# Kernel optimization log

Hardware: AMD Instinct MI355X
Metric: run time of the kernel (lower is better)

Reference implementation:

```python
import jax, jax.numpy as jnp
import numpy as np

B, M, NV, P = 4, 30000, 300000, 32
CIN, CBEV, NH = 128, 256, 4
HY, WX = 180, 180            # downsampled BEV grid (1440/8)
XSP, YSP, ZSP = 1440, 1440, 40
PC_MIN = np.array([-75.2, -75.2, -2.0], np.float32)
PC_SIZE = np.array([150.4, 150.4, 6.0], np.float32)


def setup_inputs() -> dict:
    key = jax.random.key(0)
    ks = jax.random.split(key, 20)
    w = lambda i, shape: jax.random.normal(ks[i], shape, jnp.float32) * 0.02

    voxel_features = jax.random.normal(ks[0], (NV, CIN), jnp.float32)
    b = jax.random.randint(ks[1], (NV,), 0, B)
    z = jax.random.randint(ks[2], (NV,), 0, ZSP)
    y = jax.random.randint(ks[3], (NV,), 0, YSP)
    x = jax.random.randint(ks[4], (NV,), 0, XSP)
    sp_indices = jnp.stack([b, z, y, x], -1).astype(jnp.int32)  # [NV,4] (b,z,y,x)

    # unique downsampled BEV cells -> deterministic scatter_nd
    cells = jax.random.permutation(ks[5], B * HY * WX)[:M]
    nb = cells // (HY * WX)
    rem = cells % (HY * WX)
    new_indices = jnp.stack([nb, jnp.zeros_like(nb), rem // WX, rem % WX], -1).astype(jnp.int32)

    ki = jax.random.randint(ks[6], (M, P), 0, NV)
    drop = jax.random.uniform(ks[7], (M, P)) < 0.3
    drop = drop.at[:, 0].set(False)  # at least one valid neighbor per query
    key_indices = jnp.where(drop, -1, ki).astype(jnp.int32)

    bev = jax.random.normal(ks[8], (B, CBEV, HY, WX), jnp.float32)

    return {
        'voxel_features': voxel_features, 'sp_indices': sp_indices,
        'new_indices': new_indices, 'key_indices': key_indices, 'bev': bev,
        'w_pos': w(9, (CIN, 3)), 'b_pos': jnp.zeros((CIN,), jnp.float32),
        'w_bev': w(10, (CIN, CBEV)), 'b_bev': jnp.zeros((CIN,), jnp.float32),
        'g_q': jnp.ones((CIN,), jnp.float32), 'be_q': jnp.zeros((CIN,), jnp.float32),
        'g_k': jnp.ones((CIN,), jnp.float32), 'be_k': jnp.zeros((CIN,), jnp.float32),
        'g_f': jnp.ones((CIN,), jnp.float32), 'be_f': jnp.zeros((CIN,), jnp.float32),
        'w_in': w(11, (3 * CIN, CIN)), 'b_in': jnp.zeros((3 * CIN,), jnp.float32),
        'w_out': w(12, (CIN, CIN)), 'b_out': jnp.zeros((CIN,), jnp.float32),
        'w_fc1': w(13, (CIN, CIN)), 'b_fc1': jnp.zeros((CIN,), jnp.float32),
        'w_fc2': w(14, (CIN, CIN)), 'b_fc2': jnp.zeros((CIN,), jnp.float32),
    }


def _ln(x, g, b):
    m = jnp.mean(x, -1, keepdims=True)
    v = jnp.mean((x - m) ** 2, -1, keepdims=True)
    return (x - m) * jax.lax.rsqrt(v + 1e-5) * g + b


def reference(voxel_features, sp_indices, new_indices, key_indices, bev,
              w_pos, b_pos, w_bev, b_bev, g_q, be_q, g_k, be_k, g_f, be_f,
              w_in, b_in, w_out, b_out, w_fc1, b_fc1, w_fc2, b_fc2):
    gelu = lambda t: jax.nn.gelu(t, approximate=False)
    key_mask = key_indices < 0            # [M,P] True -> padded neighbor
    safe = jnp.clip(key_indices, 0)

    key_feats = voxel_features[safe]      # [M,P,CIN] gather (grouping_operation)

    # voxel-center coords (with_coords), xyz order from indices[:, [3,2,1]]
    vs_sp = jnp.asarray(PC_SIZE / np.array([XSP, YSP, ZSP], np.float32))
    sp_coords = (sp_indices[:, jnp.array([3, 2, 1])].astype(jnp.float32) + 0.5) * vs_sp + jnp.asarray(PC_MIN)
    key_coords = sp_coords[safe]          # [M,P,3]
    vs_new = jnp.asarray(PC_SIZE / np.array([HY, WX, 1], np.float32))
    que_coords = (new_indices[:, jnp.array([3, 2, 1])].astype(jnp.float32) + 0.5) * vs_new + jnp.asarray(PC_MIN)
    key_coords = key_coords - que_coords[:, None, :]   # use_relative_coords

    # positional embedding: Conv1d(3, CIN, 1) == linear over coord dim, + GELU
    key_feats = key_feats + gelu(key_coords @ w_pos.T + b_pos)

    # dense BEV gather at downsampled voxel locations
    bev_hw = jnp.transpose(bev, (0, 2, 3, 1))           # [B,HY,WX,CBEV]
    bev_feats = bev_hw[new_indices[:, 0], new_indices[:, 2], new_indices[:, 3]]  # [M,CBEV]

    shortcut = gelu(bev_feats @ w_bev.T + b_bev)        # [M,CIN]  bev_proj
    q = _ln(shortcut, g_q, be_q)
    k = _ln(key_feats, g_k, be_k)                       # [M,P,CIN]

    C, dh = CIN, CIN // NH
    wq, wk, wv = w_in[:C], w_in[C:2 * C], w_in[2 * C:]
    bq, bk, bv = b_in[:C], b_in[C:2 * C], b_in[2 * C:]
    m = q.shape[0]
    qh = (q @ wq.T + bq).reshape(m, NH, dh)             # query seq-len 1 per voxel
    kh = (k @ wk.T + bk).reshape(m, P, NH, dh)
    vh = (k @ wv.T + bv).reshape(m, P, NH, dh)
    scale = jnp.float32(1.0 / np.sqrt(dh))
    logits = jnp.einsum('mhd,mphd->mhp', qh, kh) * scale
    logits = jnp.where(key_mask[:, None, :], -jnp.inf, logits)  # key_padding_mask
    attn = jax.nn.softmax(logits, -1)
    av = jnp.einsum('mhp,mphd->mhd', attn, vh).reshape(m, C)
    attend = av @ w_out.T + b_out

    xf = attend + shortcut
    yf = _ln(xf, g_f, be_f)
    yf = gelu(yf @ w_fc1.T + b_fc1) @ w_fc2.T + b_fc2   # MLP
    feats = yf + xf                                     # [M,CIN]

    # densify: scatter_nd into [B, z=1, HY, WX, C] then -> [B, C, HY, WX]
    dense = jnp.zeros((B, HY, WX, C), feats.dtype)
    dense = dense.at[new_indices[:, 0], new_indices[:, 2], new_indices[:, 3]].set(feats)
    return jnp.transpose(dense, (0, 3, 1, 2))
```

## Files before the change

### kernel.cpp

```cpp
#include <hip/hip_runtime.h>
#include <hip/hip_bf16.h>
#include <cmath>

#define C_IN 128
#define NKEY 32
#define N_H 4
#define D_H 32
#define C_BEV 256
#define H_Y 180
#define W_X 180

typedef __attribute__((ext_vector_type(8))) short short8;
typedef __attribute__((ext_vector_type(4))) float f32x4;

__device__ __forceinline__ float gelu_fast(float x) {
    const float y2 = fminf(1.5957691216057308f * (x + 0.044715f * x * x * x), 80.0f);
    const float e = __expf(y2);
    return x * e / (e + 1.0f);
}
__device__ __forceinline__ float dot4(float4 a, float4 b) {
    return a.x * b.x + a.y * b.y + a.z * b.z + a.w * b.w;
}
__device__ __forceinline__ float bf2f(ushort u) {
    union { unsigned int i; float f; } c; c.i = ((unsigned int)u) << 16; return c.f;
}
__device__ __forceinline__ ushort f2bf(float x) {
    __hip_bfloat16 h = __float2bfloat16(x);
    return *reinterpret_cast<ushort*>(&h);
}

__global__ void conv_swz(const float* __restrict__ src, ushort* __restrict__ dst,
                         int K, int total) {
    const int idx = blockIdx.x * 256 + threadIdx.x;
    if (idx < total) {
        const int j = idx & 7;
        const int t8 = idx >> 3;
        const int lane = t8 & 63;
        const int tile = t8 >> 6;
        const int NK = K >> 5;
        const int kt = tile % NK, ct = tile / NK;
        const int row = ct * 16 + (lane & 15);
        const int k = kt * 32 + (lane >> 4) * 8 + j;
        dst[idx] = f2bf(src[(size_t)row * K + k]);
    }
}

__global__ void conv_swz_t(const float* __restrict__ w_in, ushort* __restrict__ dst) {
    const int idx = blockIdx.x * 256 + threadIdx.x;
    if (idx < 16384) {
        const int j = idx & 7;
        const int lane = (idx >> 3) & 63;
        const int tile = idx >> 9;
        const int ct = tile & 7, h = tile >> 3;
        const int row_w = 128 + h * 32 + (lane >> 4) * 8 + j;
        const int col = ct * 16 + (lane & 15);
        dst[idx] = f2bf(w_in[(size_t)row_w * C_IN + col]);
    }
}

__global__ void build_inv(const int* __restrict__ ni, int* __restrict__ inv, int M) {
    const int m = blockIdx.x * 256 + threadIdx.x;
    if (m < M) {
        const int b = ni[m*4+0], y = ni[m*4+2], x = ni[m*4+3];
        inv[(b * H_Y + y) * W_X + x] = m;
    }
}

__global__ __launch_bounds__(256) void compact_bev(
    const float* __restrict__ bev, const int* __restrict__ inv,
    float* __restrict__ pack)
{
    const int bid = blockIdx.x;
    const int xr = bid % 12;
    const int y  = (bid / 12) % H_Y;
    const int b  = bid / (12 * H_Y);
    const int x0 = xr * 16;
    const int width = (x0 + 16 <= W_X) ? 16 : (W_X - x0);
    const int tid = threadIdx.x;

    __shared__ float tile[16][257];

    const int xq = (tid & 3) * 4;
    #pragma unroll
    for (int p = 0; p < 4; ++p) {
        const int c = p * 64 + (tid >> 2);
        if (xq < width) {
            const float4 v = *(const float4*)(bev +
                (((size_t)b * C_BEV + c) * H_Y + y) * W_X + x0 + xq);
            tile[xq+0][c] = v.x; tile[xq+1][c] = v.y;
            tile[xq+2][c] = v.z; tile[xq+3][c] = v.w;
        }
    }
    __syncthreads();
    for (int xi = 0; xi < width; ++xi) {
        const int m = inv[(b * H_Y + y) * W_X + x0 + xi];
        if (m >= 0) pack[(size_t)m * C_BEV + tid] = tile[xi][tid];
    }
}

__global__ __launch_bounds__(256) void write_out_t(
    const int* __restrict__ inv, const float* __restrict__ featbuf,
    float* __restrict__ out)
{
    const int bid = blockIdx.x;
    const int xr = bid % 12;
    const int y  = (bid / 12) % H_Y;
    const int b  = bid / (12 * H_Y);
    const int x0 = xr * 16;
    const int width = (x0 + 16 <= W_X) ? 16 : (W_X - x0);
    const int tid = threadIdx.x;

    __shared__ float tile[16][C_IN + 1];
    __shared__ int m16[16];

    if (tid < 16) m16[tid] = (tid < width) ? inv[(b * H_Y + y) * W_X + x0 + tid] : -1;
    __syncthreads();

    #pragma unroll
    for (int pass = 0; pass < 8; ++pass) {
        const int xi = pass * 2 + (tid >> 7);
        const int c  = tid & 127;
        const int m  = m16[xi];
        tile[xi][c] = (m >= 0) ? featbuf[(size_t)m * C_IN + c] : 0.0f;
    }
    __syncthreads();

    #pragma unroll
    for (int pass = 0; pass < 8; ++pass) {
        const int c  = pass * 16 + (tid >> 4);
        const int xi = tid & 15;
        if (xi < width)
            out[(((size_t)b * C_IN + c) * H_Y + y) * W_X + x0 + xi] = tile[xi][c];
    }
}

__global__ __launch_bounds__(256) void k_pre(
    float* __restrict__ pack, const ushort* __restrict__ wbev_s,
    const float* __restrict__ b_bev, const float* __restrict__ g_q,
    const float* __restrict__ be_q, const ushort* __restrict__ wq_s,
    const ushort* __restrict__ wkt_s, const float* __restrict__ b_in,
    float* __restrict__ sc_g, float* __restrict__ tbvbuf, const int M)
{
    __shared__ ushort bevl16[16][C_BEV + 8];
    __shared__ float  scl[16][C_IN];
    __shared__ ushort qlnl16[16][C_IN + 8];
    __shared__ ushort qhl16[16][C_IN + 8];
    __shared__ ushort tl16[16][N_H][C_IN];
    const int tid = threadIdx.x;
    const int m16 = blockIdx.x * 16;
    const int wave = tid >> 6, lane = tid & 63;
    const int llo = lane & 15, lhi = lane >> 4;
    const int qs = tid >> 4, seg = tid & 15;
    int mq = m16 + qs; if (mq >= M) mq = M - 1;

    {
        const float4* srcp = (const float4*)(pack + (size_t)mq * C_BEV + seg * 16);
        ushort tmp[16];
        #pragma unroll
        for (int j4 = 0; j4 < 4; ++j4) {
            const float4 v = srcp[j4];
            tmp[j4*4+0] = f2bf(v.x); tmp[j4*4+1] = f2bf(v.y);
            tmp[j4*4+2] = f2bf(v.z); tmp[j4*4+3] = f2bf(v.w);
        }
        short8* d = (short8*)&bevl16[qs][seg * 16];
        d[0] = *(short8*)&tmp[0];
        d[1] = *(short8*)&tmp[8];
    }
    __syncthreads();

    {
        f32x4 acc0 = {0.f,0.f,0.f,0.f}, acc1 = {0.f,0.f,0.f,0.f};
        #pragma unroll
        for (int kt = 0; kt < 8; ++kt) {
            const short8 a = *(const short8*)&bevl16[llo][kt*32 + lhi*8];
            const short8 b0 = *(const short8*)&wbev_s[(size_t)(((wave    )*8 + kt)*64 + lane)*8];
            const short8 b1 = *(const short8*)&wbev_s[(size_t)(((wave + 4)*8 + kt)*64 + lane)*8];
            acc0 = __builtin_amdgcn_mfma_f32_16x16x32_bf16(a, b0, acc0, 0, 0, 0);
            acc1 = __builtin_amdgcn_mfma_f32_16x16x32_bf16(a, b1, acc1, 0, 0, 0);
        }
        #pragma unroll
        for (int qe = 0; qe < 4; ++qe) {
            const int row = lhi * 4 + qe;
            const int c0 = wave * 16 + llo, c1 = (wave + 4) * 16 + llo;
            scl[row][c0] = gelu_fast(acc0[qe] + b_bev[c0]);
            scl[row][c1] = gelu_fast(acc1[qe] + b_bev[c1]);
        }
    }
    __syncthreads();

    {
        float* dst = sc_g + (size_t)mq * C_IN + seg * 8;
        float v[8];
        #pragma unroll
        for (int j = 0; j < 8; ++j) v[j] = scl[qs][seg * 8 + j];
        *(float4*)&dst[0] = make_float4(v[0], v[1], v[2], v[3]);
        *(float4*)&dst[4] = make_float4(v[4], v[5], v[6], v[7]);

        float s = 0.f;
        #pragma unroll
        for (int j = 0; j < 8; ++j) s += v[j];
        s += __shfl_xor(s, 1); s += __shfl_xor(s, 2);
        s += __shfl_xor(s, 4); s += __shfl_xor(s, 8);
        const float mean = s * (1.0f / 128.0f);
        float vv = 0.f;
        #pragma unroll
        for (int j = 0; j < 8; ++j) { const float d = v[j] - mean; vv += d * d; }
        vv += __shfl_xor(vv, 1); vv += __shfl_xor(vv, 2);
        vv += __shfl_xor(vv, 4); vv += __shfl_xor(vv, 8);
        const float rs = rsqrtf(vv * (1.0f / 128.0f) + 1e-5f);
        #pragma unroll
        for (int j = 0; j < 8; ++j) {
            const int c = seg * 8 + j;
            qlnl16[qs][c] = f2bf((v[j] - mean) * rs * g_q[c] + be_q[c]);
        }
    }
    __syncthreads();

    {
        f32x4 acc0 = {0.f,0.f,0.f,0.f}, acc1 = {0.f,0.f,0.f,0.f};
        #pragma unroll
        for (int kt = 0; kt < 4; ++kt) {
            const short8 a = *(const short8*)&qlnl16[llo][kt*32 + lhi*8];
            const short8 b0 = *(const short8*)&wq_s[(size_t)(((wave    )*4 + kt)*64 + lane)*8];
            const short8 b1 = *(const short8*)&wq_s[(size_t)(((wave + 4)*4 + kt)*64 + lane)*8];
            acc0 = __builtin_amdgcn_mfma_f32_16x16x32_bf16(a, b0, acc0, 0, 0, 0);
            acc1 = __builtin_amdgcn_mfma_f32_16x16x32_bf16(a, b1, acc1, 0, 0, 0);
        }
        #pragma unroll
        for (int qe = 0; qe < 4; ++qe) {
            const int row = lhi * 4 + qe;
            const int c0 = wave * 16 + llo, c1 = (wave + 4) * 16 + llo;
            const float v0 = acc0[qe] + b_in[c0];
            const float v1 = acc1[qe] + b_in[c1];
            scl[row][c0] = v0;  qhl16[row][c0] = f2bf(v0);
            scl[row][c1] = v1;  qhl16[row][c1] = f2bf(v1);
        }
    }
    __syncthreads();

    {
        #pragma unroll
        for (int h = 0; h < N_H; ++h) {
            const short8 a = *(const short8*)&qhl16[llo][h*32 + lhi*8];
            #pragma unroll
            for (int cti = 0; cti < 2; ++cti) {
                const int ct = wave + cti * 4;
                const short8 b = *(const short8*)&wkt_s[(size_t)(((h*8 + ct)*64 + lane))*8];
                f32x4 acc = {0.f,0.f,0.f,0.f};
                acc = __builtin_amdgcn_mfma_f32_16x16x32_bf16(a, b, acc, 0, 0, 0);
                #pragma unroll
                for (int qe = 0; qe < 4; ++qe)
                    tl16[lhi*4 + qe][h][ct*16 + llo] = f2bf(acc[qe]);
            }
        }
    }
    __syncthreads();

    {
        ushort* dstu = (ushort*)(pack + (size_t)mq * C_BEV);
        const ushort* srcu = &tl16[qs][0][0];
        #pragma unroll
        for (int j8 = 0; j8 < 4; ++j8)
            *(short8*)&dstu[seg*32 + j8*8] = *(const short8*)&srcu[seg*32 + j8*8];

        const int h = seg >> 2, quarter = seg & 3;
        float part = 0.f;
        #pragma unroll
        for (int j = 0; j < 8; ++j) {
            const int d = h*32 + quarter*8 + j;
            part += scl[qs][d] * b_in[C_IN + d];
        }
        part += __shfl_xor(part, 1);
        part += __shfl_xor(part, 2);
        if (quarter == 0) tbvbuf[(size_t)mq * 4 + h] = part;
    }
}

__global__ __launch_bounds__(512) void k_attn(
    const float* __restrict__ vf, const int* __restrict__ spi,
    const int* __restrict__ ni, const int* __restrict__ kidx,
    float* __restrict__ pack, const float* __restrict__ tbvbuf,
    const float* __restrict__ w_pos, const float* __restrict__ b_pos,
    const float* __restrict__ g_k, const float* __restrict__ be_k,
    const ushort* __restrict__ wv_s, const float* __restrict__ b_in,
    const int M)
{
    const int tid = threadIdx.x;
    const int m2 = blockIdx.x * 2;
    const int mA = m2;
    const int mB = (m2 + 1 < M) ? (m2 + 1) : (M - 1);

    __shared__ ushort kf16[64][C_IN + 8];
    __shared__ ushort t16[2][N_H][C_IN + 8];
    __shared__ float  Sl[2][NKEY][4];
    __shared__ float  attnw[2 * 4 * NKEY];
    __shared__ ushort kbarA16[16][C_IN + 8];
    __shared__ float  tbvs[8];
    __shared__ int    kmsk[64];
    __shared__ int    kvs[64];
    __shared__ int    lst[64];
    __shared__ int    cntS;
    __shared__ float  prm[768];

    const int wave = tid >> 6, lane = tid & 63;
    const int llo = lane & 15, lhi = lane >> 4;
    const int nxA = ni[mA*4+3], nyA = ni[mA*4+2];
    const int nxB = ni[mB*4+3], nyB = ni[mB*4+2];

    for (int i = tid; i < 768; i += 512) {
        float val;
        if (i < 384)      val = w_pos[i];
        else if (i < 512) val = b_pos[i - 384];
        else if (i < 640) val = g_k[i - 512];
        else              val = be_k[i - 640];
        prm[i] = val;
    }
    {
        const int q = tid >> 8, rem = tid & 255;
        const int h = rem >> 6, c2 = rem & 63;
        const uint u = ((const uint*)(pack + (size_t)(q ? mB : mA) * C_BEV))[rem];
        ((uint*)&t16[q][h][0])[c2] = u;
    }
    if (tid < 8) tbvs[tid] = tbvbuf[(size_t)((tid >> 2) ? mB : mA) * 4 + (tid & 3)];
    if (tid < 64) {
        const int qk = tid >> 5;
        const int kv = kidx[(size_t)(qk ? mB : mA) * NKEY + (tid & 31)];
        const bool act = (kv >= 0);
        kmsk[tid] = act ? 0 : 1;
        kvs[tid]  = act ? kv : 0;
        const unsigned long long bal = __ballot(act);
        if (tid == 0) cntS = (int)__popcll(bal);
        if (act) lst[(int)__popcll(bal & ((1ull << tid) - 1ull))] = tid;
    }
    __syncthreads();

    {
        const int grp = tid >> 3, g = tid & 7, c0 = g * 16;
        if (kmsk[grp]) {
            const short8 z = (short8){0,0,0,0,0,0,0,0};
            short8* d = (short8*)&kf16[grp][c0];
            d[0] = z; d[1] = z;
        }
        if (grp < cntS) {
            const int kk = lst[grp];
            const int qk = kk >> 5;
            const int safe = kvs[kk];
            const int nxk = qk ? nxB : nxA, nyk = qk ? nyB : nyA;
            const float qxk = (nxk + 0.5f) * (150.4f / 180.0f) - 75.2f;
            const float qyk = (nyk + 0.5f) * (150.4f / 180.0f) - 75.2f;
            const int sz = spi[safe * 4 + 1];
            const int sy = spi[safe * 4 + 2];
            const int sx = spi[safe * 4 + 3];
            const float cx = (sx + 0.5f) * (150.4f / 1440.0f) - 75.2f - qxk;
            const float cy = (sy + 0.5f) * (150.4f / 1440.0f) - 75.2f - qyk;
            const float cz = (sz + 0.5f) * (6.0f / 40.0f)     - 3.0f;

            float v[16];
            const float4* src = (const float4*)(vf + (size_t)safe * C_IN + c0);
            #pragma unroll
            for (int j = 0; j < 4; ++j) {
                float4 t = src[j];
                v[j*4+0] = t.x; v[j*4+1] = t.y; v[j*4+2] = t.z; v[j*4+3] = t.w;
            }
            #pragma unroll
            for (int ch = 0; ch < 2; ++ch) {
                const int cb = c0 + ch * 8;
                float wpl[24];
                const float4* wpr = (const float4*)&prm[cb * 3];
                #pragma unroll
                for (int j4 = 0; j4 < 6; ++j4) *(float4*)&wpl[j4*4] = wpr[j4];
                float bpl[8];
                *(float4*)&bpl[0] = *(const float4*)&prm[384 + cb];
                *(float4*)&bpl[4] = *(const float4*)&prm[384 + cb + 4];
                #pragma unroll
                for (int j = 0; j < 8; ++j) {
                    const float e = cx*wpl[j*3+0] + cy*wpl[j*3+1] + cz*wpl[j*3+2] + bpl[j];
                    v[ch*8+j] += gelu_fast(e);
                }
            }
            float s = 0.f;
            #pragma unroll
            for (int j = 0; j < 16; ++j) s += v[j];
            s += __shfl_xor(s, 1); s += __shfl_xor(s, 2); s += __shfl_xor(s, 4);
            const float mean = s * (1.0f / 128.0f);
            float vv = 0.f;
            #pragma unroll
            for (int j = 0; j < 16; ++j) { const float d = v[j] - mean; vv += d * d; }
            vv += __shfl_xor(vv, 1); vv += __shfl_xor(vv, 2); vv += __shfl_xor(vv, 4);
            const float rs = rsqrtf(vv * (1.0f / 128.0f) + 1e-5f);
            ushort o[16];
            #pragma unroll
            for (int ch = 0; ch < 2; ++ch) {
                const int cb = c0 + ch * 8;
                float gkl[8], bel[8];
                *(float4*)&gkl[0] = *(const float4*)&prm[512 + cb];
                *(float4*)&gkl[4] = *(const float4*)&prm[512 + cb + 4];
                *(float4*)&bel[0] = *(const float4*)&prm[640 + cb];
                *(float4*)&bel[4] = *(const float4*)&prm[640 + cb + 4];
                #pragma unroll
                for (int j = 0; j < 8; ++j)
                    o[ch*8+j] = f2bf((v[ch*8+j] - mean) * rs * gkl[j] + bel[j]);
            }
            short8* drow = (short8*)(&kf16[kk][c0]);
            drow[0] = *(short8*)&o[0];
            drow[1] = *(short8*)&o[8];
        }
    }
    __syncthreads();

    if (wave < 4) {
        const int q = wave >> 1, rt = wave & 1;
        f32x4 acc = {0.f,0.f,0.f,0.f};
        #pragma unroll
        for (int kt = 0; kt < 4; ++kt) {
            const short8 a = *(const short8*)&kf16[q*NKEY + rt*16 + llo][kt*32 + lhi*8];
            const short8 b = *(const short8*)&t16[q][llo & 3][kt*32 + lhi*8];
            acc = __builtin_amdgcn_mfma_f32_16x16x32_bf16(a, b, acc, 0, 0, 0);
        }
        if (llo < 4) {
            #pragma unroll
            for (int qe = 0; qe < 4; ++qe)
                Sl[q][rt*16 + lhi*4 + qe][llo] = acc[qe];
        }
    } else {
        const int idx = (wave - 4) * 64 + lane;
        uint* zb = (uint*)&kbarA16[8][0];
        if (idx < 544) zb[idx] = 0;
        if (idx + 256 < 544) zb[idx + 256] = 0;
    }
    __syncthreads();

    if (tid < 256) {
        const int q = tid >> 7, h = (tid >> 5) & 3, p = tid & 31;
        const int msk = kmsk[q*NKEY + p];
        float logit = msk ? -3.0e38f
                          : (Sl[q][p][h] + tbvs[q*4 + h]) * 0.17677669529663687f;
        float mx = logit;
        #pragma unroll
        for (int o = 16; o >= 1; o >>= 1) mx = fmaxf(mx, __shfl_xor(mx, o));
        const float e = msk ? 0.0f : __expf(logit - mx);
        float ssum = e;
        #pragma unroll
        for (int o = 16; o >= 1; o >>= 1) ssum += __shfl_xor(ssum, o);
        attnw[(q*4 + h)*32 + p] = e / ssum;
    }
    __syncthreads();

    {
        const int q = tid >> 8, r = tid & 255;
        const int c = r & 127, h2 = r >> 7;
        #pragma unroll
        for (int hi = 0; hi < 2; ++hi) {
            const int hh = h2 + 2 * hi;
            float acc = 0.f;
            #pragma unroll
            for (int p = 0; p < NKEY; ++p)
                acc += attnw[(q*4 + hh)*32 + p] * bf2f(kf16[q*NKEY + p][c]);
            kbarA16[q*4 + hh][c] = f2bf(acc);
        }
    }
    __syncthreads();

    {
        const int ct = wave;
        const int h = ct >> 1;
        f32x4 acc = {0.f,0.f,0.f,0.f};
        #pragma unroll
        for (int kt = 0; kt < 4; ++kt) {
            const short8 a = *(const short8*)&kbarA16[llo][kt*32 + lhi*8];
            const short8 b = *(const short8*)&wv_s[(size_t)(((ct*4 + kt)*64 + lane))*8];
            acc = __builtin_amdgcn_mfma_f32_16x16x32_bf16(a, b, acc, 0, 0, 0);
        }
        if (lhi < 2) {
            const int q = lhi;
            const int j = ct * 16 + llo;
            if ((m2 + q) < M)
                pack[(size_t)(q ? mB : mA) * C_BEV + C_IN + j] = acc[h] + b_in[2*C_IN + j];
        }
    }
}

__global__ __launch_bounds__(256) void k_post(
    const float* __restrict__ pack,
    const ushort* __restrict__ wout_s, const float* __restrict__ b_out,
    const float* __restrict__ g_f, const float* __restrict__ be_f,
    const ushort* __restrict__ wfc1_s, const float* __restrict__ b_fc1,
    const ushort* __restrict__ wfc2_s, const float* __restrict__ b_fc2,
    float* __restrict__ scfeat, const int M)
{
    __shared__ ushort avl16[16][C_IN + 8];
    __shared__ float  sclp[16][C_IN];
    __shared__ float  xfl[16][C_IN];
    __shared__ ushort ylnl16[16][C_IN + 8];
    __shared__ ushort h1l16[16][C_IN + 8];
    const int tid = threadIdx.x;
    const int m16 = blockIdx.x * 16;
    const int wave = tid >> 6, lane = tid & 63;
    const int llo = lane & 15, lhi = lane >> 4;
    const int qs = tid >> 4, seg = tid & 15;
    int mq = m16 + qs; if (mq >= M) mq = M - 1;

    {
        const float4* ap = (const float4*)(pack + (size_t)mq * C_BEV + C_IN + seg * 8);
        const float4 a0 = ap[0], a1 = ap[1];
        ushort tmp[8];
        tmp[0]=f2bf(a0.x); tmp[1]=f2bf(a0.y); tmp[2]=f2bf(a0.z); tmp[3]=f2bf(a0.w);
        tmp[4]=f2bf(a1.x); tmp[5]=f2bf(a1.y); tmp[6]=f2bf(a1.z); tmp[7]=f2bf(a1.w);
        *(short8*)&avl16[qs][seg * 8] = *(short8*)&tmp[0];
        const float4* sp = (const float4*)(scfeat + (size_t)mq * C_IN + seg * 8);
        *(float4*)&sclp[qs][seg * 8]     = sp[0];
        *(float4*)&sclp[qs][seg * 8 + 4] = sp[1];
    }
    __syncthreads();

    {
        f32x4 acc0 = {0.f,0.f,0.f,0.f}, acc1 = {0.f,0.f,0.f,0.f};
        #pragma unroll
        for (int kt = 0; kt < 4; ++kt) {
            const short8 a = *(const short8*)&avl16[llo][kt*32 + lhi*8];
            const short8 b0 = *(const short8*)&wout_s[(size_t)(((wave    )*4 + kt)*64 + lane)*8];
            const short8 b1 = *(const short8*)&wout_s[(size_t)(((wave + 4)*4 + kt)*64 + lane)*8];
            acc0 = __builtin_amdgcn_mfma_f32_16x16x32_bf16(a, b0, acc0, 0, 0, 0);
            acc1 = __builtin_amdgcn_mfma_f32_16x16x32_bf16(a, b1, acc1, 0, 0, 0);
        }
        #pragma unroll
        for (int qe = 0; qe < 4; ++qe) {
            const int row = lhi * 4 + qe;
            const int c0 = wave * 16 + llo, c1 = (wave + 4) * 16 + llo;
            xfl[row][c0] = acc0[qe] + b_out[c0] + sclp[row][c0];
            xfl[row][c1] = acc1[qe] + b_out[c1] + sclp[row][c1];
        }
    }
    __syncthreads();

    {
        float v[8];
        #pragma unroll
        for (int j = 0; j < 8; ++j) v[j] = xfl[qs][seg * 8 + j];
        float s = 0.f;
        #pragma unroll
        for (int j = 0; j < 8; ++j) s += v[j];
        s += __shfl_xor(s, 1); s += __shfl_xor(s, 2);
        s += __shfl_xor(s, 4); s += __shfl_xor(s, 8);
        const float mean = s * (1.0f / 128.0f);
        float vv = 0.f;
        #pragma unroll
        for (int j = 0; j < 8; ++j) { const float d = v[j] - mean; vv += d * d; }
        vv += __shfl_xor(vv, 1); vv += __shfl_xor(vv, 2);
        vv += __shfl_xor(vv, 4); vv += __shfl_xor(vv, 8);
        const float rs = rsqrtf(vv * (1.0f / 128.0f) + 1e-5f);
        #pragma unroll
        for (int j = 0; j < 8; ++j) {
            const int c = seg * 8 + j;
            ylnl16[qs][c] = f2bf((v[j] - mean) * rs * g_f[c] + be_f[c]);
        }
    }
    __syncthreads();

    {
        f32x4 acc0 = {0.f,0.f,0.f,0.f}, acc1 = {0.f,0.f,0.f,0.f};
        #pragma unroll
        for (int kt = 0; kt < 4; ++kt) {
            const short8 a = *(const short8*)&ylnl16[llo][kt*32 + lhi*8];
            const short8 b0 = *(const short8*)&wfc1_s[(size_t)(((wave    )*4 + kt)*64 + lane)*8];
            const short8 b1 = *(const short8*)&wfc1_s[(size_t)(((wave + 4)*4 + kt)*64 + lane)*8];
            acc0 = __builtin_amdgcn_mfma_f32_16x16x32_bf16(a, b0, acc0, 0, 0, 0);
            acc1 = __builtin_amdgcn_mfma_f32_16x16x32_bf16(a, b1, acc1, 0, 0, 0);
        }
        #pragma unroll
        for (int qe = 0; qe < 4; ++qe) {
            const int row = lhi * 4 + qe;
            const int c0 = wave * 16 + llo, c1 = (wave + 4) * 16 + llo;
            h1l16[row][c0] = f2bf(gelu_fast(acc0[qe] + b_fc1[c0]));
            h1l16[row][c1] = f2bf(gelu_fast(acc1[qe] + b_fc1[c1]));
        }
    }
    __syncthreads();

    {
        f32x4 acc0 = {0.f,0.f,0.f,0.f}, acc1 = {0.f,0.f,0.f,0.f};
        #pragma unroll
        for (int kt = 0; kt < 4; ++kt) {
            const short8 a = *(const short8*)&h1l16[llo][kt*32 + lhi*8];
            const short8 b0 = *(const short8*)&wfc2_s[(size_t)(((wave    )*4 + kt)*64 + lane)*8];
            const short8 b1 = *(const short8*)&wfc2_s[(size_t)(((wave + 4)*4 + kt)*64 + lane)*8];
            acc0 = __builtin_amdgcn_mfma_f32_16x16x32_bf16(a, b0, acc0, 0, 0, 0);
            acc1 = __builtin_amdgcn_mfma_f32_16x16x32_bf16(a, b1, acc1, 0, 0, 0);
        }
        #pragma unroll
        for (int qe = 0; qe < 4; ++qe) {
            const int row = lhi * 4 + qe;
            const int c0 = wave * 16 + llo, c1 = (wave + 4) * 16 + llo;
            sclp[row][c0] = acc0[qe] + b_fc2[c0] + xfl[row][c0];
            sclp[row][c1] = acc1[qe] + b_fc2[c1] + xfl[row][c1];
        }
    }
    __syncthreads();

    {
        float* dst = scfeat + (size_t)mq * C_IN + seg * 8;
        *(float4*)&dst[0] = make_float4(sclp[qs][seg*8+0], sclp[qs][seg*8+1],
                                        sclp[qs][seg*8+2], sclp[qs][seg*8+3]);
        *(float4*)&dst[4] = make_float4(sclp[qs][seg*8+4], sclp[qs][seg*8+5],
                                        sclp[qs][seg*8+6], sclp[qs][seg*8+7]);
    }
}

extern "C" void kernel_launch(void* const* d_in, const int* in_sizes, int n_in,
                              void* d_out, int out_size, void* d_ws, size_t ws_size,
                              hipStream_t stream) {
    const float* vf    = (const float*)d_in[0];
    const int*   spi   = (const int*)  d_in[1];
    const int*   ni    = (const int*)  d_in[2];
    const int*   kidx  = (const int*)  d_in[3];
    const float* bev   = (const float*)d_in[4];
    const float* w_pos = (const float*)d_in[5];
    const float* b_pos = (const float*)d_in[6];
    const float* w_bev = (const float*)d_in[7];
    const float* b_bev = (const float*)d_in[8];
    const float* g_q   = (const float*)d_in[9];
    const float* be_q  = (const float*)d_in[10];
    const float* g_k   = (const float*)d_in[11];
    const float* be_k  = (const float*)d_in[12];
    const float* g_f   = (const float*)d_in[13];
    const float* be_f  = (const float*)d_in[14];
    const float* w_in  = (const float*)d_in[15];
    const float* b_in  = (const float*)d_in[16];
    const float* w_out = (const float*)d_in[17];
    const float* b_out = (const float*)d_in[18];
    const float* w_fc1 = (const float*)d_in[19];
    const float* b_fc1 = (const float*)d_in[20];
    const float* w_fc2 = (const float*)d_in[21];
    const float* b_fc2 = (const float*)d_in[22];
    float* out = (float*)d_out;

    const int M = in_sizes[3] / NKEY;

    char* ws = (char*)d_ws;
    const size_t MiB = 1u << 20;
    int*    inv    = (int*)ws;
    float*  tbvbuf = (float*)(ws + 2 * MiB);
    float*  pack   = (float*)(ws + 4 * MiB);
    float*  scfeat = (float*)(ws + 34 * MiB);
    ushort* wbev_s = (ushort*)(ws + 49 * MiB);
    ushort* wq_s   = wbev_s + 128 * 256;
    ushort* wout_s = wq_s   + 128 * 128;
    ushort* wfc1_s = wout_s + 128 * 128;
    ushort* wfc2_s = wfc1_s + 128 * 128;
    ushort* wkt_s  = wfc2_s + 128 * 128;
    ushort* wv_s   = wkt_s  + 16384;

    hipMemsetAsync(inv, 0xFF, (size_t)4 * H_Y * W_X * sizeof(int), stream);
    build_inv<<<(M + 255) / 256, 256, 0, stream>>>(ni, inv, M);

    conv_swz<<<128, 256, 0, stream>>>(w_bev, wbev_s, C_BEV, 128 * 256);
    conv_swz<<<64, 256, 0, stream>>>(w_in,  wq_s,   C_IN, 128 * 128);
    conv_swz<<<64, 256, 0, stream>>>(w_out, wout_s, C_IN, 128 * 128);
    conv_swz<<<64, 256, 0, stream>>>(w_fc1, wfc1_s, C_IN, 128 * 128);
    conv_swz<<<64, 256, 0, stream>>>(w_fc2, wfc2_s, C_IN, 128 * 128);
    conv_swz_t<<<64, 256, 0, stream>>>(w_in, wkt_s);
    conv_swz<<<64, 256, 0, stream>>>(w_in + 2 * C_IN * C_IN, wv_s, C_IN, 128 * 128);

    compact_bev<<<4 * H_Y * 12, 256, 0, stream>>>(bev, inv, pack);

    k_pre<<<(M + 15) / 16, 256, 0, stream>>>(pack, wbev_s, b_bev, g_q, be_q,
                                             wq_s, wkt_s, b_in, scfeat, tbvbuf, M);
    k_attn<<<(M + 1) / 2, 512, 0, stream>>>(vf, spi, ni, kidx, pack, tbvbuf,
                                            w_pos, b_pos, g_k, be_k, wv_s, b_in, M);
    k_post<<<(M + 15) / 16, 256, 0, stream>>>(pack, wout_s, b_out, g_f, be_f,
                                              wfc1_s, b_fc1, wfc2_s, b_fc2, scfeat, M);

    write_out_t<<<4 * H_Y * 12, 256, 0, stream>>>(inv, scfeat, out);
}
```

Measured before the change: 328.0 us.

## Process four queries per attention block instead of two

```diff
diff --git a/kernel.cpp b/kernel.cpp
--- a/kernel.cpp
+++ b/kernel.cpp
@@ -27,6 +27,11 @@
 __device__ __forceinline__ ushort f2bf(float x) {
     __hip_bfloat16 h = __float2bfloat16(x);
     return *reinterpret_cast<ushort*>(&h);
+}
+__device__ __forceinline__ void bfpair(uint u, float& lo, float& hi) {
+    union { uint i; float f; } a, b;
+    a.i = u << 16; b.i = u & 0xffff0000u;
+    lo = a.f; hi = b.f;
 }
 
 __global__ void conv_swz(const float* __restrict__ src, ushort* __restrict__ dst,
@@ -286,26 +291,25 @@
     const int M)
 {
     const int tid = threadIdx.x;
-    const int m2 = blockIdx.x * 2;
-    const int mA = m2;
-    const int mB = (m2 + 1 < M) ? (m2 + 1) : (M - 1);
-
-    __shared__ ushort kf16[64][C_IN + 8];
-    __shared__ ushort t16[2][N_H][C_IN + 8];
-    __shared__ float  Sl[2][NKEY][4];
-    __shared__ float  attnw[2 * 4 * NKEY];
+    const int m4 = blockIdx.x * 4;
+    int mI[4];
+    #pragma unroll
+    for (int q = 0; q < 4; ++q) mI[q] = (m4 + q < M) ? (m4 + q) : (M - 1);
+
+    __shared__ ushort kf16[4 * NKEY][C_IN + 8];
+    __shared__ ushort t16[4][N_H][C_IN + 8];
+    __shared__ float  Sl[4][NKEY][4];
+    __shared__ float  attnw[4 * 4 * NKEY];
     __shared__ ushort kbarA16[16][C_IN + 8];
-    __shared__ float  tbvs[8];
-    __shared__ int    kmsk[64];
-    __shared__ int    kvs[64];
-    __shared__ int    lst[64];
-    __shared__ int    cntS;
+    __shared__ float  tbvs[16];
+    __shared__ int    kmsk[128];
+    __shared__ int    kvs[128];
+    __shared__ int    lst[2][64];
+    __shared__ int    cntS[2];
     __shared__ float  prm[768];
 
     const int wave = tid >> 6, lane = tid & 63;
     const int llo = lane & 15, lhi = lane >> 4;
-    const int nxA = ni[mA*4+3], nyA = ni[mA*4+2];
-    const int nxB = ni[mB*4+3], nyB = ni[mB*4+2];
 
     for (int i = tid; i < 768; i += 512) {
         float val;
@@ -316,36 +320,44 @@
         prm[i] = val;
     }
     {
-        const int q = tid >> 8, rem = tid & 255;
-        const int h = rem >> 6, c2 = rem & 63;
-        const uint u = ((const uint*)(pack + (size_t)(q ? mB : mA) * C_BEV))[rem];
-        ((uint*)&t16[q][h][0])[c2] = u;
-    }
-    if (tid < 8) tbvs[tid] = tbvbuf[(size_t)((tid >> 2) ? mB : mA) * 4 + (tid & 3)];
-    if (tid < 64) {
-        const int qk = tid >> 5;
-        const int kv = kidx[(size_t)(qk ? mB : mA) * NKEY + (tid & 31)];
+        const int q = tid >> 7, rem = tid & 127;
+        const uint* srcu = (const uint*)(pack + (size_t)mI[q] * C_BEV);
+        #pragma unroll
+        for (int j = 0; j < 2; ++j) {
+            const int u = rem * 2 + j;
+            const int h = u >> 6, c2 = u & 63;
+            ((uint*)&t16[q][h][0])[c2] = srcu[u];
+        }
+    }
+    if (tid < 16) tbvs[tid] = tbvbuf[(size_t)mI[tid >> 2] * 4 + (tid & 3)];
+    if (tid < 128) {
+        const int half = tid >> 6;
+        const int row = tid;
+        const int q = row >> 5;
+        const int kv = kidx[(size_t)mI[q] * NKEY + (row & 31)];
         const bool act = (kv >= 0);
-        kmsk[tid] = act ? 0 : 1;
-        kvs[tid]  = act ? kv : 0;
+        kmsk[row] = act ? 0 : 1;
+        kvs[row]  = act ? kv : 0;
         const unsigned long long bal = __ballot(act);
-        if (tid == 0) cntS = (int)__popcll(bal);
-        if (act) lst[(int)__popcll(bal & ((1ull << tid) - 1ull))] = tid;
-    }
-    __syncthreads();
-
-    {
+        if ((tid & 63) == 0) cntS[half] = (int)__popcll(bal);
+        if (act) lst[half][(int)__popcll(bal & ((1ull << (tid & 63)) - 1ull))] = row;
+    }
+    __syncthreads();
+
+    #pragma unroll
+    for (int it = 0; it < 2; ++it) {
         const int grp = tid >> 3, g = tid & 7, c0 = g * 16;
-        if (kmsk[grp]) {
+        const int rowz = it * 64 + grp;
+        if (kmsk[rowz]) {
             const short8 z = (short8){0,0,0,0,0,0,0,0};
-            short8* d = (short8*)&kf16[grp][c0];
+            short8* d = (short8*)&kf16[rowz][c0];
             d[0] = z; d[1] = z;
         }
-        if (grp < cntS) {
-            const int kk = lst[grp];
+        if (grp < cntS[it]) {
+            const int kk = lst[it][grp];
             const int qk = kk >> 5;
             const int safe = kvs[kk];
-            const int nxk = qk ? nxB : nxA, nyk = qk ? nyB : nyA;
+            const int nxk = ni[mI[qk]*4+3], nyk = ni[mI[qk]*4+2];
             const float qxk = (nxk + 0.5f) * (150.4f / 180.0f) - 75.2f;
             const float qyk = (nyk + 0.5f) * (150.4f / 180.0f) - 75.2f;
             const int sz = spi[safe * 4 + 1];
@@ -408,7 +420,7 @@
     }
     __syncthreads();
 
-    if (wave < 4) {
+    {
         const int q = wave >> 1, rt = wave & 1;
         f32x4 acc = {0.f,0.f,0.f,0.f};
         #pragma unroll
@@ -422,15 +434,10 @@
             for (int qe = 0; qe < 4; ++qe)
                 Sl[q][rt*16 + lhi*4 + qe][llo] = acc[qe];
         }
-    } else {
-        const int idx = (wave - 4) * 64 + lane;
-        uint* zb = (uint*)&kbarA16[8][0];
-        if (idx < 544) zb[idx] = 0;
-        if (idx + 256 < 544) zb[idx + 256] = 0;
-    }
-    __syncthreads();
-
-    if (tid < 256) {
+    }
+    __syncthreads();
+
+    {
         const int q = tid >> 7, h = (tid >> 5) & 3, p = tid & 31;
         const int msk = kmsk[q*NKEY + p];
         float logit = msk ? -3.0e38f
@@ -447,16 +454,24 @@
     __syncthreads();
 
     {
-        const int q = tid >> 8, r = tid & 255;
-        const int c = r & 127, h2 = r >> 7;
+        const int q = tid >> 7, rest = tid & 127;
+        const int hp = rest >> 6, c2 = rest & 63;
         #pragma unroll
         for (int hi = 0; hi < 2; ++hi) {
-            const int hh = h2 + 2 * hi;
-            float acc = 0.f;
-            #pragma unroll
-            for (int p = 0; p < NKEY; ++p)
-                acc += attnw[(q*4 + hh)*32 + p] * bf2f(kf16[q*NKEY + p][c]);
-            kbarA16[q*4 + hh][c] = f2bf(acc);
+            const int h = hp * 2 + hi;
+            const float* aw = &attnw[(q*4 + h)*32];
+            float accL = 0.f, accH = 0.f;
+            #pragma unroll
+            for (int p = 0; p < NKEY; ++p) {
+                const uint u = ((const uint*)&kf16[q*NKEY + p][0])[c2];
+                float lo, hi2;
+                bfpair(u, lo, hi2);
+                const float w = aw[p];
+                accL += w * lo;
+                accH += w * hi2;
+            }
+            kbarA16[q*4 + h][c2*2]     = f2bf(accL);
+            kbarA16[q*4 + h][c2*2 + 1] = f2bf(accH);
         }
     }
     __syncthreads();
@@ -471,12 +486,9 @@
             const short8 b = *(const short8*)&wv_s[(size_t)(((ct*4 + kt)*64 + lane))*8];
             acc = __builtin_amdgcn_mfma_f32_16x16x32_bf16(a, b, acc, 0, 0, 0);
         }
-        if (lhi < 2) {
-            const int q = lhi;
-            const int j = ct * 16 + llo;
-            if ((m2 + q) < M)
-                pack[(size_t)(q ? mB : mA) * C_BEV + C_IN + j] = acc[h] + b_in[2*C_IN + j];
-        }
+        const int j = ct * 16 + llo;
+        if ((m4 + lhi) < M)
+            pack[(size_t)mI[lhi] * C_BEV + C_IN + j] = acc[h] + b_in[2*C_IN + j];
     }
 }
 
@@ -665,7 +677,7 @@
 
     k_pre<<<(M + 15) / 16, 256, 0, stream>>>(pack, wbev_s, b_bev, g_q, be_q,
                                              wq_s, wkt_s, b_in, scfeat, tbvbuf, M);
-    k_attn<<<(M + 1) / 2, 512, 0, stream>>>(vf, spi, ni, kidx, pack, tbvbuf,
+    k_attn<<<(M + 3) / 4, 512, 0, stream>>>(vf, spi, ni, kidx, pack, tbvbuf,
                                             w_pos, b_pos, g_k, be_k, wv_s, b_in, M);
     k_post<<<(M + 15) / 16, 256, 0, stream>>>(pack, wout_s, b_out, g_f, be_f,
                                               wfc1_s, b_fc1, wfc2_s, b_fc2, scfeat, M);
```

After: 343.7 us. 4.8% more time.
